# Performance work log

Measured on AMD Instinct MI355X. Metric: run time of the kernel, lower is better.

The kernel has to match this reference:

```python
import jax, jax.numpy as jnp
import numpy as np

B, S, W, V, E, H, T = 512, 512, 3, 100000, 128, 100, 64
PAD = 0


def setup_inputs() -> dict:
    key = jax.random.key(0)
    ks = jax.random.split(key, 10)
    inputs = jax.random.randint(ks[0], (B, S, W), 0, V)          # word feature ids
    tags = jax.random.randint(ks[1], (B, S), 0, T)
    emb_table = jax.random.normal(ks[2], (V, E), jnp.float32) * 0.1
    W1 = jax.random.normal(ks[3], (E, H), jnp.float32) * (1.0 / np.sqrt(E))
    b1 = jnp.zeros((H,), jnp.float32)
    W2 = jax.random.normal(ks[4], (H, T), jnp.float32) * (1.0 / np.sqrt(H))
    b2 = jnp.zeros((T,), jnp.float32)
    start_trans = jax.random.uniform(ks[5], (T,), jnp.float32, -0.1, 0.1)
    end_trans = jax.random.uniform(ks[6], (T,), jnp.float32, -0.1, 0.1)
    transitions = jax.random.uniform(ks[7], (T, T), jnp.float32, -0.1, 0.1)
    return {"inputs": inputs, "tags": tags, "emb_table": emb_table,
            "W1": W1, "b1": b1, "W2": W2, "b2": b2,
            "start_trans": start_trans, "end_trans": end_trans,
            "transitions": transitions}


def reference(inputs, tags, emb_table, W1, b1, W2, b2,
              start_trans, end_trans, transitions):
    # mask: token is real if any word feature != padding_idx. [S,B] (time-major)
    mask = (jnp.sum(inputs != PAD, axis=-1) != 0).T
    # Emission scorer (dropout disabled = eval/deterministic)
    emb = jnp.take(emb_table, inputs, axis=0).sum(axis=2)        # [B,S,E]
    h = jnp.tanh(emb @ W1 + b1)                                  # [B,S,H]
    em = (h @ W2 + b2).transpose(1, 0, 2)                        # [S,B,T]
    tags_t = tags.T                                              # [S,B]
    maskf = mask.astype(em.dtype)
    b_idx = jnp.arange(em.shape[1])

    # ---- numerator: score of the gold tag path ----
    score = start_trans[tags_t[0]] + em[0, b_idx, tags_t[0]]     # [B]
    trans_sc = transitions[tags_t[:-1], tags_t[1:]]              # [S-1,B]
    em_sc = jnp.take_along_axis(em[1:], tags_t[1:, :, None], axis=2)[..., 0]
    score = score + jnp.sum((trans_sc + em_sc) * maskf[1:], axis=0)
    seq_ends = jnp.sum(mask.astype(jnp.int32), axis=0) - 1       # [B]
    last_tags = tags_t[seq_ends, b_idx]
    numerator = score + end_trans[last_tags]

    # ---- denominator: log partition via forward algorithm (log-semiring scan) ----
    alpha0 = start_trans[None, :] + em[0]                        # [B,T]

    def step(alpha, x):
        em_t, m_t = x                                            # [B,T], [B]
        nxt = jax.nn.logsumexp(
            alpha[:, :, None] + transitions[None, :, :] + em_t[:, None, :],
            axis=1)                                              # [B,T]
        return jnp.where(m_t[:, None], nxt, alpha), None

    alpha, _ = jax.lax.scan(step, alpha0, (em[1:], mask[1:]))
    denominator = jax.nn.logsumexp(alpha + end_trans[None, :], axis=1)

    # loss = -log-likelihood, per batch element (reduce=False)
    return denominator - numerator
```

## Files before the change

kernel.cpp:

```cpp
#include <hip/hip_runtime.h>

#define B_ 512
#define S_ 512
#define E_ 128
#define H_ 100
#define T_ 64
#define V_ 100000
#define BS_ (B_*S_)

typedef __attribute__((ext_vector_type(8))) short bf16x8;
typedef __attribute__((ext_vector_type(4))) float f32x4;
typedef _Float16 h2 __attribute__((ext_vector_type(2)));
union U16x4 { uint4 u; bf16x8 s; };

__device__ __forceinline__ unsigned f2bf1(float x){
    unsigned u = __float_as_uint(x);
    return (u + 0x7FFFu + ((u>>16)&1u)) >> 16;
}
__device__ __forceinline__ float bf2f(unsigned short h){
    return __uint_as_float(((unsigned)h)<<16);
}
__device__ __forceinline__ float rfl_f(float x){
    return __uint_as_float(__builtin_amdgcn_readfirstlane(__float_as_uint(x)));
}
__device__ __forceinline__ unsigned addpack3(unsigned a, unsigned b, unsigned c){
    float lo = __uint_as_float(a<<16) + __uint_as_float(b<<16) + __uint_as_float(c<<16);
    float hi = __uint_as_float(a&0xFFFF0000u) + __uint_as_float(b&0xFFFF0000u)
             + __uint_as_float(c&0xFFFF0000u);
    return f2bf1(lo) | (f2bf1(hi)<<16);
}
__device__ __forceinline__ float fdot2h(unsigned u, h2 e, float c){
    h2 p; __builtin_memcpy(&p, &u, 4);
#if __has_builtin(__builtin_amdgcn_fdot2)
    return __builtin_amdgcn_fdot2(p, e, c, false);
#else
    return fmaf((float)p.x, (float)e.x, fmaf((float)p.y, (float)e.y, c));
#endif
}
__device__ __forceinline__ float dpp_xor1(float x){
    return __int_as_float(__builtin_amdgcn_mov_dpp(__float_as_int(x), 0xB1, 0xF, 0xF, true));
}
__device__ __forceinline__ float dpp_xor2(float x){
    return __int_as_float(__builtin_amdgcn_mov_dpp(__float_as_int(x), 0x4E, 0xF, 0xF, true));
}

__global__ __launch_bounds__(256) void prep_tbl(
    const float* __restrict__ tbl, uint2* __restrict__ tblh)
{
    int idx = blockIdx.x*256 + threadIdx.x;
    if (idx < (V_*E_)/4) {
        float4 v = ((const float4*)tbl)[idx];
        uint2 o;
        o.x = f2bf1(v.x) | (f2bf1(v.y)<<16);
        o.y = f2bf1(v.z) | (f2bf1(v.w)<<16);
        tblh[idx] = o;
    }
}

__global__ __launch_bounds__(64) void prep_w(
    const float* __restrict__ W1, const float* __restrict__ W2,
    uint4* __restrict__ W1f, uint4* __restrict__ W2f)
{
    const int idx = blockIdx.x*64 + threadIdx.x;
    if (idx < 7*4*64) {
        int lane = idx & 63, kt = (idx>>6)&3, nt = idx>>8;
        int n = nt*16 + (lane&15);
        int kb = kt*32 + (lane>>4)*8;
        unsigned wv[4];
        #pragma unroll
        for (int p = 0; p < 4; ++p) {
            float v0 = (n < H_) ? W1[(kb+2*p  )*H_ + n] : 0.f;
            float v1 = (n < H_) ? W1[(kb+2*p+1)*H_ + n] : 0.f;
            wv[p] = f2bf1(v0) | (f2bf1(v1) << 16);
        }
        W1f[idx] = make_uint4(wv[0],wv[1],wv[2],wv[3]);
    } else {
        int id2 = idx - 7*4*64;
        int lane = id2 & 63, kt = (id2>>6)&3, nt = id2>>8;
        int n = nt*16 + (lane&15);
        int kb = kt*32 + (lane>>4)*8;
        unsigned wv[4];
        #pragma unroll
        for (int p = 0; p < 4; ++p) {
            int k0 = kb+2*p, k1 = kb+2*p+1;
            float v0 = (k0 < H_) ? W2[k0*T_ + n] : 0.f;
            float v1 = (k1 < H_) ? W2[k1*T_ + n] : 0.f;
            wv[p] = f2bf1(v0) | (f2bf1(v1) << 16);
        }
        W2f[id2] = make_uint4(wv[0],wv[1],wv[2],wv[3]);
    }
}

__global__ __launch_bounds__(128)
__attribute__((amdgpu_waves_per_eu(1, 1)))
void fused_kernel(
    const int* __restrict__ inputs, const int* __restrict__ tags,
    const unsigned short* __restrict__ tblh,
    const float* __restrict__ b1, const float* __restrict__ b2,
    const uint4* __restrict__ W1f, const uint4* __restrict__ W2f,
    const float* __restrict__ start_trans, const float* __restrict__ end_trans,
    const float* __restrict__ trans, float* __restrict__ out)
{
    __shared__ uint4 sW1f[1792];
    __shared__ uint4 sW2f[1024];
    __shared__ __align__(16) unsigned short ring[2][4][512];
    __shared__ uint4 sA2[2][256];
    __shared__ __align__(16) _Float16 pbufH[2][T_];
    __shared__ float pubB[T_];
    __shared__ float fnum[2];
    __shared__ int   icnt[2];
    __shared__ float lsB_sh;

    const int b   = blockIdx.x;
    const int tid = threadIdx.x;
    const int w   = tid >> 6;
    const int j   = tid & 63;
    const int col = j & 15;
    const int hi  = j >> 4;
    const int rowin = hi * 4;
    const int qg  = j >> 2;
    const int qm  = j & 3;
    const bool qb0 = (j & 1) != 0;
    const bool qb1 = (j & 2) != 0;
    const int* tags_b = tags + b*S_;
    const int* in_b   = inputs + (size_t)b*S_*3;

    for (int i = tid; i < 1792; i += 128) sW1f[i] = W1f[i];
    for (int i = tid; i < 1024; i += 128) sW2f[i] = W2f[i];

    unsigned long long mball[4];
    #pragma unroll
    for (int g4 = 0; g4 < 4; ++g4) {
        int t = (w*4 + g4)*64 + j;
        int a0 = in_b[t*3+0], a1 = in_b[t*3+1], a2 = in_b[t*3+2];
        mball[g4] = __ballot((a0 | a1 | a2) != 0);
    }
    int cnt = 0;
    #pragma unroll
    for (int g4 = 0; g4 < 4; ++g4) cnt += __popcll(mball[g4]);
    if (j == 0) icnt[w] = cnt;
    if (w == 0) mball[0] &= ~1ull;

    __syncthreads();

    float bv1[7], bv2[4];
    #pragma unroll
    for (int nt = 0; nt < 7; ++nt) { int n = nt*16+col; bv1[nt] = (n < H_) ? b1[n] : 0.f; }
    #pragma unroll
    for (int nt2 = 0; nt2 < 4; ++nt2) bv2[nt2] = b2[nt2*16+col];

    h2 E2[32];
    #pragma unroll
    for (int o = 0; o < 4; ++o)
        #pragma unroll
        for (int i = 0; i < 8; ++i) {
            int r0, c0, r1, c1;
            if (w == 0) { r0 = 16*qm + 2*i; c0 = 4*qg + o; r1 = r0 + 1; c1 = c0; }
            else        { r0 = 4*qg + o; c0 = 16*qm + 2*i; r1 = r0; c1 = c0 + 1; }
            h2 e; e.x = (_Float16)__expf(trans[r0*T_ + c0]);
                  e.y = (_Float16)__expf(trans[r1*T_ + c1]);
            E2[o*8 + i] = e;
        }

    auto baseOf = [&](int p){ return w ? (480 - 16*p) : 16*p; };
    float np = 0.f;

    auto loadIdx = [&](int p, int& x, int& y, int& z){
        int t = baseOf(p) + col;
        x = in_b[t*3 + 0]; y = in_b[t*3 + 1]; z = in_b[t*3 + 2];
    };
    auto issueGathers = [&](int i0, int i1, int i2, uint4* g){
        const unsigned short* tr0 = tblh + (size_t)i0*E_;
        const unsigned short* tr1 = tblh + (size_t)i1*E_;
        const unsigned short* tr2 = tblh + (size_t)i2*E_;
        #pragma unroll
        for (int kt = 0; kt < 4; ++kt) {
            int off = kt*32 + hi*8;
            g[kt*3+0] = *(const uint4*)(tr0 + off);
            g[kt*3+1] = *(const uint4*)(tr1 + off);
            g[kt*3+2] = *(const uint4*)(tr2 + off);
        }
    };

    auto produce = [&](int p, const uint4* g){
        U16x4 a[4];
        #pragma unroll
        for (int kt = 0; kt < 4; ++kt)
            a[kt].u = make_uint4(
                addpack3(g[kt*3+0].x, g[kt*3+1].x, g[kt*3+2].x),
                addpack3(g[kt*3+0].y, g[kt*3+1].y, g[kt*3+2].y),
                addpack3(g[kt*3+0].z, g[kt*3+1].z, g[kt*3+2].z),
                addpack3(g[kt*3+0].w, g[kt*3+1].w, g[kt*3+2].w));

        f32x4 acc1[7];
        #pragma unroll
        for (int nt = 0; nt < 7; ++nt) {
            f32x4 c; c[0]=bv1[nt]; c[1]=bv1[nt]; c[2]=bv1[nt]; c[3]=bv1[nt];
            #pragma unroll
            for (int k = 0; k < 4; ++k) {
                U16x4 bfr; bfr.u = sW1f[(nt*4+k)*64 + j];
                c = __builtin_amdgcn_mfma_f32_16x16x32_bf16(a[k].s, bfr.s, c, 0,0,0);
            }
            acc1[nt] = c;
        }
        #pragma unroll
        for (int nt = 0; nt < 7; ++nt)
            #pragma unroll
            for (int rr = 0; rr < 4; ++rr) {
                float x = acc1[nt][rr];
                acc1[nt][rr] = 1.f - 2.f/(__expf(2.f*x)+1.f);
            }

        if (j >= 32) sA2[w][3*64 + j] = make_uint4(0,0,0,0);
        unsigned short* A2h = (unsigned short*)sA2[w];
        #pragma unroll
        for (int nt = 0; nt < 7; ++nt)
            #pragma unroll
            for (int rr = 0; rr < 4; ++rr) {
                int k2 = nt*16 + col;
                int kt2 = k2 >> 5, g2 = (k2>>3)&3, i2v = k2&7;
                int u4idx = kt2*64 + g2*16 + (rowin + rr);
                A2h[u4idx*8 + i2v] = (unsigned short)f2bf1(acc1[nt][rr]);
            }
        __builtin_amdgcn_wave_barrier();

        U16x4 a2[4];
        #pragma unroll
        for (int k = 0; k < 4; ++k) a2[k].u = sA2[w][k*64 + j];
        __builtin_amdgcn_wave_barrier();

        unsigned short* tbuf = (unsigned short*)sA2[w];
        #pragma unroll
        for (int nt2 = 0; nt2 < 4; ++nt2) {
            f32x4 c; c[0]=bv2[nt2]; c[1]=bv2[nt2]; c[2]=bv2[nt2]; c[3]=bv2[nt2];
            #pragma unroll
            for (int k = 0; k < 4; ++k) {
                U16x4 bfr; bfr.u = sW2f[(nt2*4+k)*64 + j];
                c = __builtin_amdgcn_mfma_f32_16x16x32_bf16(a2[k].s, bfr.s, c, 0,0,0);
            }
            #pragma unroll
            for (int rr = 0; rr < 4; ++rr)
                tbuf[(rowin+rr)*72 + nt2*16 + col] = (unsigned short)f2bf1(c[rr]);
        }
        __builtin_amdgcn_wave_barrier();

        {
            const int rl = j >> 2;
            const int ch = (j & 3) * 2;
            const uint4* t4 = (const uint4*)tbuf;
            uint4 u0 = t4[rl*9 + ch];
            uint4 u1 = t4[rl*9 + ch + 1];
            int row = baseOf(p) + rl;
            int grp = row >> 3;
            int kidx = w ? (63 - grp) : grp;
            uint4* dst = (uint4*)&ring[w][kidx & 3][(row & 7)*64];
            dst[ch]   = u0;
            dst[ch+1] = u1;
        }
        __builtin_amdgcn_wave_barrier();

        if (j < 16) {
            int t = baseOf(p) + j;
            if (t >= 1) {
                int word = (t >> 6) - w*4;
                if ((mball[word] >> (t & 63)) & 1ull) {
                    int tp = tags_b[t-1], tc = tags_b[t];
                    int grp = t >> 3;
                    int kidx = w ? (63 - grp) : grp;
                    np += trans[tp*T_ + tc] + bf2f(ring[w][kidx & 3][(t & 7)*64 + tc]);
                }
            }
        }
    };

    uint4 g[12];
    int i0, i1, i2, ni0, ni1, ni2;
    loadIdx(0, i0, i1, i2);
    issueGathers(i0, i1, i2, g);
    produce(0, g);
    float a, ls;
    if (w == 0) {
        if (j == 0) {
            int tag0 = tags_b[0];
            np += start_trans[tag0] + bf2f(ring[0][0][tag0]);
        }
        float x0v = start_trans[j] + bf2f(ring[0][0][j]);
        ls = rfl_f(x0v);
        a  = __expf(x0v - ls);
    } else {
        a  = __expf(end_trans[j]);
        ls = 0.f;
    }
    loadIdx(1, i0, i1, i2);
    issueGathers(i0, i1, i2, g);
    produce(1, g);
    loadIdx(2, i0, i1, i2);
    issueGathers(i0, i1, i2, g);
    loadIdx(3, ni0, ni1, ni2);

    float eg[8];
    #pragma unroll
    for (int s = 0; s < 8; ++s)
        eg[s] = __expf(bf2f(ring[w][0][(w ? (7-s) : s)*64 + j]));

    for (int p = 0; p < 16; ++p) {
        #pragma unroll
        for (int kk = 0; kk < 2; ++kk) {
            const int k = 2*p + kk;
            unsigned short raw16[8];
            if (k < 31) {
                const unsigned short* nxt = ring[w][(k+1) & 3];
                #pragma unroll
                for (int s = 0; s < 8; ++s)
                    raw16[s] = nxt[(w ? (7-s) : s)*64 + j];
            }
            const int ag = w ? (63 - k) : k;
            const unsigned mg = (unsigned)((mball[(ag>>3) - w*4] >> ((ag&7)*8)) & 0xFFull);

            #pragma unroll
            for (int s = 0; s < 8; ++s) {
                float wv = (w == 0) ? a : (eg[s] * a);
                pbufH[w][j] = (_Float16)(wv * 0.015625f);
                __builtin_amdgcn_wave_barrier();
                float sc   = rfl_f(a);
                float sinv = __builtin_amdgcn_rcpf(sc);
                float logs = __logf(sc);
                float keep = a * sinv;
                float dmul = ((w == 0) ? (eg[s] * sinv) : sinv) * 64.0f;

                const uint4* ph = (const uint4*)pbufH[w];
                uint4 U0 = ph[2*qm];
                uint4 U1 = ph[2*qm + 1];
                float p0, p1, p2, p3;
                p0 = fdot2h(U0.x, E2[ 0], 0.f);  p0 = fdot2h(U0.y, E2[ 1], p0);
                p0 = fdot2h(U0.z, E2[ 2], p0);   p0 = fdot2h(U0.w, E2[ 3], p0);
                p0 = fdot2h(U1.x, E2[ 4], p0);   p0 = fdot2h(U1.y, E2[ 5], p0);
                p0 = fdot2h(U1.z, E2[ 6], p0);   p0 = fdot2h(U1.w, E2[ 7], p0);
                p1 = fdot2h(U0.x, E2[ 8], 0.f);  p1 = fdot2h(U0.y, E2[ 9], p1);
                p1 = fdot2h(U0.z, E2[10], p1);   p1 = fdot2h(U0.w, E2[11], p1);
                p1 = fdot2h(U1.x, E2[12], p1);   p1 = fdot2h(U1.y, E2[13], p1);
                p1 = fdot2h(U1.z, E2[14], p1);   p1 = fdot2h(U1.w, E2[15], p1);
                p2 = fdot2h(U0.x, E2[16], 0.f);  p2 = fdot2h(U0.y, E2[17], p2);
                p2 = fdot2h(U0.z, E2[18], p2);   p2 = fdot2h(U0.w, E2[19], p2);
                p2 = fdot2h(U1.x, E2[20], p2);   p2 = fdot2h(U1.y, E2[21], p2);
                p2 = fdot2h(U1.z, E2[22], p2);   p2 = fdot2h(U1.w, E2[23], p2);
                p3 = fdot2h(U0.x, E2[24], 0.f);  p3 = fdot2h(U0.y, E2[25], p3);
                p3 = fdot2h(U0.z, E2[26], p3);   p3 = fdot2h(U0.w, E2[27], p3);
                p3 = fdot2h(U1.x, E2[28], p3);   p3 = fdot2h(U1.y, E2[29], p3);
                p3 = fdot2h(U1.z, E2[30], p3);   p3 = fdot2h(U1.w, E2[31], p3);

                float t0 = qb1 ? p2 : p0;
                float t1 = qb1 ? p3 : p1;
                float s0 = qb1 ? p0 : p2;
                float s1 = qb1 ? p1 : p3;
                t0 += dpp_xor2(s0);
                t1 += dpp_xor2(s1);
                float tt = qb0 ? t1 : t0;
                float ss = qb0 ? t0 : t1;
                float y  = tt + dpp_xor1(ss);

                float cand = y * dmul;
                const int bit = (w == 0) ? s : (7 - s);
                a = ((mg >> bit) & 1u) ? cand : keep;
                ls += logs;
                __builtin_amdgcn_wave_barrier();
            }
            if (k < 31) {
                #pragma unroll
                for (int s = 0; s < 8; ++s) eg[s] = __expf(bf2f(raw16[s]));
            }
        }
        if (p <= 13) produce(p + 2, g);
        if (p <= 12) {
            issueGathers(ni0, ni1, ni2, g);
            if (p <= 11) loadIdx(p + 4, ni0, ni1, ni2);
        }
    }

    #pragma unroll
    for (int off = 32; off >= 1; off >>= 1) np += __shfl_xor(np, off, 64);
    if (j == 0) fnum[w] = np;

    if (w == 1) {
        pubB[j] = a;
        if (j == 0) lsB_sh = ls;
    }
    __syncthreads();
    if (w == 0) {
        float x = a * pubB[j];
        #pragma unroll
        for (int off = 32; off >= 1; off >>= 1) x += __shfl_xor(x, off, 64);
        int mcount = icnt[0] + icnt[1];
        int se = mcount - 1; if (se < 0) se = 0;
        const int last_tag = tags_b[se];
        float numer = fnum[0] + fnum[1] + end_trans[last_tag];
        if (j == 0) out[b] = ls + lsB_sh + __logf(x) - numer;
    }
}

extern "C" void kernel_launch(void* const* d_in, const int* in_sizes, int n_in,
                              void* d_out, int out_size, void* d_ws, size_t ws_size,
                              hipStream_t stream) {
    const int*   inputs      = (const int*)  d_in[0];
    const int*   tags        = (const int*)  d_in[1];
    const float* emb_table   = (const float*)d_in[2];
    const float* W1          = (const float*)d_in[3];
    const float* b1          = (const float*)d_in[4];
    const float* W2          = (const float*)d_in[5];
    const float* b2          = (const float*)d_in[6];
    const float* start_trans = (const float*)d_in[7];
    const float* end_trans   = (const float*)d_in[8];
    const float* transitions = (const float*)d_in[9];
    float* out = (float*)d_out;

    unsigned short* tblh = (unsigned short*)d_ws;
    uint4* W1f = (uint4*)((char*)d_ws + (size_t)V_*E_*2);
    uint4* W2f = W1f + 7*4*64;

    prep_tbl<<<dim3((V_*E_/4 + 255)/256), dim3(256), 0, stream>>>(emb_table, (uint2*)tblh);
    prep_w<<<dim3((7*4*64 + 4*4*64)/64), dim3(64), 0, stream>>>(W1, W2, W1f, W2f);
    fused_kernel<<<dim3(B_), dim3(128), 0, stream>>>(
        inputs, tags, tblh, b1, b2, W1f, W2f,
        start_trans, end_trans, transitions, out);
}
```

Before: 222.7 us.

## Split fused CRF kernel into producer and consumer waves with LDS flag handshake

The block grows from two to four waves. Two producer waves compute emissions (gather plus both MLP layers) into a deeper 8-slot LDS ring, and two consumer waves run the forward and backward log-semiring scans. The waves synchronize through spin-waited shared-memory progress flags. Before, each wave interleaved its own emission production with its scan steps. The intent is to take emission latency off the serial scan critical path, at the cost of spin-wait overhead, extra LDS, and a register budget now capped by 256-thread launch bounds with two blocks per CU.

```diff
diff --git a/kernel.cpp b/kernel.cpp
--- a/kernel.cpp
+++ b/kernel.cpp
@@ -91,8 +91,7 @@
     }
 }
 
-__global__ __launch_bounds__(128)
-__attribute__((amdgpu_waves_per_eu(1, 1)))
+__global__ __launch_bounds__(256, 2)
 void fused_kernel(
     const int* __restrict__ inputs, const int* __restrict__ tags,
     const unsigned short* __restrict__ tblh,
@@ -103,232 +102,254 @@
 {
     __shared__ uint4 sW1f[1792];
     __shared__ uint4 sW2f[1024];
-    __shared__ __align__(16) unsigned short ring[2][4][512];
+    __shared__ __align__(16) unsigned short ring[2][8][512];
     __shared__ uint4 sA2[2][256];
     __shared__ __align__(16) _Float16 pbufH[2][T_];
     __shared__ float pubB[T_];
     __shared__ float fnum[2];
     __shared__ int   icnt[2];
     __shared__ float lsB_sh;
+    __shared__ int   prodF[2];
+    __shared__ int   consF[2];
 
     const int b   = blockIdx.x;
     const int tid = threadIdx.x;
-    const int w   = tid >> 6;
+    const int wid = tid >> 6;
     const int j   = tid & 63;
+    const int d   = wid & 1;
+    const bool isProd = wid >= 2;
     const int col = j & 15;
     const int hi  = j >> 4;
     const int rowin = hi * 4;
-    const int qg  = j >> 2;
-    const int qm  = j & 3;
-    const bool qb0 = (j & 1) != 0;
-    const bool qb1 = (j & 2) != 0;
     const int* tags_b = tags + b*S_;
     const int* in_b   = inputs + (size_t)b*S_*3;
 
-    for (int i = tid; i < 1792; i += 128) sW1f[i] = W1f[i];
-    for (int i = tid; i < 1024; i += 128) sW2f[i] = W2f[i];
+    for (int i = tid; i < 1792; i += 256) sW1f[i] = W1f[i];
+    for (int i = tid; i < 1024; i += 256) sW2f[i] = W2f[i];
+    if (tid == 0) { prodF[0] = prodF[1] = 0; consF[0] = consF[1] = 0; }
 
     unsigned long long mball[4];
     #pragma unroll
     for (int g4 = 0; g4 < 4; ++g4) {
-        int t = (w*4 + g4)*64 + j;
+        int t = (d*4 + g4)*64 + j;
         int a0 = in_b[t*3+0], a1 = in_b[t*3+1], a2 = in_b[t*3+2];
         mball[g4] = __ballot((a0 | a1 | a2) != 0);
     }
-    int cnt = 0;
-    #pragma unroll
-    for (int g4 = 0; g4 < 4; ++g4) cnt += __popcll(mball[g4]);
-    if (j == 0) icnt[w] = cnt;
-    if (w == 0) mball[0] &= ~1ull;
+    if (isProd) {
+        int cnt = 0;
+        #pragma unroll
+        for (int g4 = 0; g4 < 4; ++g4) cnt += __popcll(mball[g4]);
+        if (j == 0) icnt[d] = cnt;
+    }
 
     __syncthreads();
 
-    float bv1[7], bv2[4];
-    #pragma unroll
-    for (int nt = 0; nt < 7; ++nt) { int n = nt*16+col; bv1[nt] = (n < H_) ? b1[n] : 0.f; }
-    #pragma unroll
-    for (int nt2 = 0; nt2 < 4; ++nt2) bv2[nt2] = b2[nt2*16+col];
-
-    h2 E2[32];
-    #pragma unroll
-    for (int o = 0; o < 4; ++o)
-        #pragma unroll
-        for (int i = 0; i < 8; ++i) {
-            int r0, c0, r1, c1;
-            if (w == 0) { r0 = 16*qm + 2*i; c0 = 4*qg + o; r1 = r0 + 1; c1 = c0; }
-            else        { r0 = 4*qg + o; c0 = 16*qm + 2*i; r1 = r0; c1 = c0 + 1; }
-            h2 e; e.x = (_Float16)__expf(trans[r0*T_ + c0]);
-                  e.y = (_Float16)__expf(trans[r1*T_ + c1]);
-            E2[o*8 + i] = e;
-        }
-
-    auto baseOf = [&](int p){ return w ? (480 - 16*p) : 16*p; };
-    float np = 0.f;
-
-    auto loadIdx = [&](int p, int& x, int& y, int& z){
-        int t = baseOf(p) + col;
-        x = in_b[t*3 + 0]; y = in_b[t*3 + 1]; z = in_b[t*3 + 2];
-    };
-    auto issueGathers = [&](int i0, int i1, int i2, uint4* g){
-        const unsigned short* tr0 = tblh + (size_t)i0*E_;
-        const unsigned short* tr1 = tblh + (size_t)i1*E_;
-        const unsigned short* tr2 = tblh + (size_t)i2*E_;
-        #pragma unroll
-        for (int kt = 0; kt < 4; ++kt) {
-            int off = kt*32 + hi*8;
-            g[kt*3+0] = *(const uint4*)(tr0 + off);
-            g[kt*3+1] = *(const uint4*)(tr1 + off);
-            g[kt*3+2] = *(const uint4*)(tr2 + off);
-        }
-    };
-
-    auto produce = [&](int p, const uint4* g){
-        U16x4 a[4];
-        #pragma unroll
-        for (int kt = 0; kt < 4; ++kt)
-            a[kt].u = make_uint4(
-                addpack3(g[kt*3+0].x, g[kt*3+1].x, g[kt*3+2].x),
-                addpack3(g[kt*3+0].y, g[kt*3+1].y, g[kt*3+2].y),
-                addpack3(g[kt*3+0].z, g[kt*3+1].z, g[kt*3+2].z),
-                addpack3(g[kt*3+0].w, g[kt*3+1].w, g[kt*3+2].w));
-
-        f32x4 acc1[7];
-        #pragma unroll
-        for (int nt = 0; nt < 7; ++nt) {
-            f32x4 c; c[0]=bv1[nt]; c[1]=bv1[nt]; c[2]=bv1[nt]; c[3]=bv1[nt];
-            #pragma unroll
-            for (int k = 0; k < 4; ++k) {
-                U16x4 bfr; bfr.u = sW1f[(nt*4+k)*64 + j];
-                c = __builtin_amdgcn_mfma_f32_16x16x32_bf16(a[k].s, bfr.s, c, 0,0,0);
-            }
-            acc1[nt] = c;
-        }
-        #pragma unroll
-        for (int nt = 0; nt < 7; ++nt)
-            #pragma unroll
-            for (int rr = 0; rr < 4; ++rr) {
-                float x = acc1[nt][rr];
-                acc1[nt][rr] = 1.f - 2.f/(__expf(2.f*x)+1.f);
-            }
-
-        if (j >= 32) sA2[w][3*64 + j] = make_uint4(0,0,0,0);
-        unsigned short* A2h = (unsigned short*)sA2[w];
-        #pragma unroll
-        for (int nt = 0; nt < 7; ++nt)
-            #pragma unroll
-            for (int rr = 0; rr < 4; ++rr) {
-                int k2 = nt*16 + col;
-                int kt2 = k2 >> 5, g2 = (k2>>3)&3, i2v = k2&7;
-                int u4idx = kt2*64 + g2*16 + (rowin + rr);
-                A2h[u4idx*8 + i2v] = (unsigned short)f2bf1(acc1[nt][rr]);
-            }
-        __builtin_amdgcn_wave_barrier();
-
-        U16x4 a2[4];
-        #pragma unroll
-        for (int k = 0; k < 4; ++k) a2[k].u = sA2[w][k*64 + j];
-        __builtin_amdgcn_wave_barrier();
-
-        unsigned short* tbuf = (unsigned short*)sA2[w];
-        #pragma unroll
-        for (int nt2 = 0; nt2 < 4; ++nt2) {
-            f32x4 c; c[0]=bv2[nt2]; c[1]=bv2[nt2]; c[2]=bv2[nt2]; c[3]=bv2[nt2];
-            #pragma unroll
-            for (int k = 0; k < 4; ++k) {
-                U16x4 bfr; bfr.u = sW2f[(nt2*4+k)*64 + j];
-                c = __builtin_amdgcn_mfma_f32_16x16x32_bf16(a2[k].s, bfr.s, c, 0,0,0);
-            }
-            #pragma unroll
-            for (int rr = 0; rr < 4; ++rr)
-                tbuf[(rowin+rr)*72 + nt2*16 + col] = (unsigned short)f2bf1(c[rr]);
-        }
-        __builtin_amdgcn_wave_barrier();
-
-        {
-            const int rl = j >> 2;
-            const int ch = (j & 3) * 2;
-            const uint4* t4 = (const uint4*)tbuf;
-            uint4 u0 = t4[rl*9 + ch];
-            uint4 u1 = t4[rl*9 + ch + 1];
-            int row = baseOf(p) + rl;
-            int grp = row >> 3;
-            int kidx = w ? (63 - grp) : grp;
-            uint4* dst = (uint4*)&ring[w][kidx & 3][(row & 7)*64];
-            dst[ch]   = u0;
-            dst[ch+1] = u1;
-        }
-        __builtin_amdgcn_wave_barrier();
-
-        if (j < 16) {
-            int t = baseOf(p) + j;
-            if (t >= 1) {
-                int word = (t >> 6) - w*4;
-                if ((mball[word] >> (t & 63)) & 1ull) {
-                    int tp = tags_b[t-1], tc = tags_b[t];
-                    int grp = t >> 3;
-                    int kidx = w ? (63 - grp) : grp;
-                    np += trans[tp*T_ + tc] + bf2f(ring[w][kidx & 3][(t & 7)*64 + tc]);
+    auto baseOf = [&](int p){ return d ? (496 - 16*p) : 16*p; };
+
+    float aF = 0.f, lsF = 0.f;
+
+    if (isProd) {
+        float bv1[7], bv2[4];
+        #pragma unroll
+        for (int nt = 0; nt < 7; ++nt) { int n = nt*16+col; bv1[nt] = (n < H_) ? b1[n] : 0.f; }
+        #pragma unroll
+        for (int nt2 = 0; nt2 < 4; ++nt2) bv2[nt2] = b2[nt2*16+col];
+
+        auto loadIdx = [&](int p, int& x, int& y, int& z){
+            int t = baseOf(p) + col;
+            x = in_b[t*3 + 0]; y = in_b[t*3 + 1]; z = in_b[t*3 + 2];
+        };
+        auto issueGathers = [&](int i0, int i1, int i2, uint4* g){
+            const unsigned short* tr0 = tblh + (size_t)i0*E_;
+            const unsigned short* tr1 = tblh + (size_t)i1*E_;
+            const unsigned short* tr2 = tblh + (size_t)i2*E_;
+            #pragma unroll
+            for (int kt = 0; kt < 4; ++kt) {
+                int off = kt*32 + hi*8;
+                g[kt*3+0] = *(const uint4*)(tr0 + off);
+                g[kt*3+1] = *(const uint4*)(tr1 + off);
+                g[kt*3+2] = *(const uint4*)(tr2 + off);
+            }
+        };
+
+        uint4 g[12];
+        int i0, i1, i2;
+        float np = 0.f;
+        loadIdx(0, i0, i1, i2);
+        issueGathers(i0, i1, i2, g);
+
+        for (int p = 0; p < 16; ++p) {
+            U16x4 a4[4];
+            #pragma unroll
+            for (int kt = 0; kt < 4; ++kt)
+                a4[kt].u = make_uint4(
+                    addpack3(g[kt*3+0].x, g[kt*3+1].x, g[kt*3+2].x),
+                    addpack3(g[kt*3+0].y, g[kt*3+1].y, g[kt*3+2].y),
+                    addpack3(g[kt*3+0].z, g[kt*3+1].z, g[kt*3+2].z),
+                    addpack3(g[kt*3+0].w, g[kt*3+1].w, g[kt*3+2].w));
+            if (p < 15) { loadIdx(p+1, i0, i1, i2); issueGathers(i0, i1, i2, g); }
+
+            f32x4 acc1[7];
+            #pragma unroll
+            for (int nt = 0; nt < 7; ++nt) {
+                f32x4 c; c[0]=bv1[nt]; c[1]=bv1[nt]; c[2]=bv1[nt]; c[3]=bv1[nt];
+                #pragma unroll
+                for (int k = 0; k < 4; ++k) {
+                    U16x4 bfr; bfr.u = sW1f[(nt*4+k)*64 + j];
+                    c = __builtin_amdgcn_mfma_f32_16x16x32_bf16(a4[k].s, bfr.s, c, 0,0,0);
                 }
-            }
-        }
-    };
-
-    uint4 g[12];
-    int i0, i1, i2, ni0, ni1, ni2;
-    loadIdx(0, i0, i1, i2);
-    issueGathers(i0, i1, i2, g);
-    produce(0, g);
-    float a, ls;
-    if (w == 0) {
-        if (j == 0) {
-            int tag0 = tags_b[0];
-            np += start_trans[tag0] + bf2f(ring[0][0][tag0]);
-        }
-        float x0v = start_trans[j] + bf2f(ring[0][0][j]);
-        ls = rfl_f(x0v);
-        a  = __expf(x0v - ls);
+                acc1[nt] = c;
+            }
+            #pragma unroll
+            for (int nt = 0; nt < 7; ++nt)
+                #pragma unroll
+                for (int rr = 0; rr < 4; ++rr) {
+                    float x = acc1[nt][rr];
+                    acc1[nt][rr] = 1.f - 2.f/(__expf(2.f*x)+1.f);
+                }
+
+            if (j >= 32) sA2[d][3*64 + j] = make_uint4(0,0,0,0);
+            unsigned short* A2h = (unsigned short*)sA2[d];
+            #pragma unroll
+            for (int nt = 0; nt < 7; ++nt)
+                #pragma unroll
+                for (int rr = 0; rr < 4; ++rr) {
+                    int k2 = nt*16 + col;
+                    int kt2 = k2 >> 5, g2 = (k2>>3)&3, i2v = k2&7;
+                    int u4idx = kt2*64 + g2*16 + (rowin + rr);
+                    A2h[u4idx*8 + i2v] = (unsigned short)f2bf1(acc1[nt][rr]);
+                }
+            __builtin_amdgcn_wave_barrier();
+
+            U16x4 a2[4];
+            #pragma unroll
+            for (int k = 0; k < 4; ++k) a2[k].u = sA2[d][k*64 + j];
+            __builtin_amdgcn_wave_barrier();
+
+            unsigned short* tbuf = (unsigned short*)sA2[d];
+            #pragma unroll
+            for (int nt2 = 0; nt2 < 4; ++nt2) {
+                f32x4 c; c[0]=bv2[nt2]; c[1]=bv2[nt2]; c[2]=bv2[nt2]; c[3]=bv2[nt2];
+                #pragma unroll
+                for (int k = 0; k < 4; ++k) {
+                    U16x4 bfr; bfr.u = sW2f[(nt2*4+k)*64 + j];
+                    c = __builtin_amdgcn_mfma_f32_16x16x32_bf16(a2[k].s, bfr.s, c, 0,0,0);
+                }
+                #pragma unroll
+                for (int rr = 0; rr < 4; ++rr)
+                    tbuf[(rowin+rr)*72 + nt2*16 + col] = (unsigned short)f2bf1(c[rr]);
+            }
+            __builtin_amdgcn_wave_barrier();
+
+            if (p >= 4) {
+                volatile int* cf = &consF[d];
+                while (*cf < 2*p - 7) __builtin_amdgcn_s_sleep(1);
+                __asm__ volatile("" ::: "memory");
+            }
+            {
+                const int rl = j >> 2;
+                const int ch = (j & 3) * 2;
+                const uint4* t4 = (const uint4*)tbuf;
+                uint4 u0 = t4[rl*9 + ch];
+                uint4 u1 = t4[rl*9 + ch + 1];
+                int row = baseOf(p) + rl;
+                int grp = row >> 3;
+                int kidx = d ? (63 - grp) : grp;
+                uint4* dst = (uint4*)&ring[d][kidx & 7][(row & 7)*64];
+                dst[ch]   = u0;
+                dst[ch+1] = u1;
+            }
+            __asm__ volatile("s_waitcnt lgkmcnt(0)" ::: "memory");
+            if (j == 0) prodF[d] = 2*p + 2;
+            __builtin_amdgcn_wave_barrier();
+
+            if (j < 16) {
+                int t = baseOf(p) + j;
+                if (t >= 1) {
+                    int word = (t >> 6) - d*4;
+                    if ((mball[word] >> (t & 63)) & 1ull) {
+                        int tp = tags_b[t-1], tc = tags_b[t];
+                        int grp = t >> 3;
+                        int kidx = d ? (63 - grp) : grp;
+                        np += trans[tp*T_ + tc] + bf2f(ring[d][kidx & 7][(t & 7)*64 + tc]);
+                    }
+                }
+            }
+            if (d == 0 && p == 0 && j == 0) {
+                int tag0 = tags_b[0];
+                np += start_trans[tag0] + bf2f(ring[0][0][tag0]);
+            }
+        }
+
+        #pragma unroll
+        for (int off = 32; off >= 1; off >>= 1) np += __shfl_xor(np, off, 64);
+        if (j == 0) fnum[d] = np;
+
     } else {
-        a  = __expf(end_trans[j]);
-        ls = 0.f;
-    }
-    loadIdx(1, i0, i1, i2);
-    issueGathers(i0, i1, i2, g);
-    produce(1, g);
-    loadIdx(2, i0, i1, i2);
-    issueGathers(i0, i1, i2, g);
-    loadIdx(3, ni0, ni1, ni2);
-
-    float eg[8];
-    #pragma unroll
-    for (int s = 0; s < 8; ++s)
-        eg[s] = __expf(bf2f(ring[w][0][(w ? (7-s) : s)*64 + j]));
-
-    for (int p = 0; p < 16; ++p) {
-        #pragma unroll
-        for (int kk = 0; kk < 2; ++kk) {
-            const int k = 2*p + kk;
+        const int qg  = j >> 2;
+        const int qm  = j & 3;
+        const bool qb0 = (j & 1) != 0;
+        const bool qb1 = (j & 2) != 0;
+
+        h2 E2[32];
+        #pragma unroll
+        for (int o = 0; o < 4; ++o)
+            #pragma unroll
+            for (int i = 0; i < 8; ++i) {
+                int r0, c0, r1, c1;
+                if (d == 0) { r0 = 16*qm + 2*i; c0 = 4*qg + o; r1 = r0 + 1; c1 = c0; }
+                else        { r0 = 4*qg + o; c0 = 16*qm + 2*i; r1 = r0; c1 = c0 + 1; }
+                h2 e; e.x = (_Float16)__expf(trans[r0*T_ + c0]);
+                      e.y = (_Float16)__expf(trans[r1*T_ + c1]);
+                E2[o*8 + i] = e;
+            }
+        if (d == 0) mball[0] &= ~1ull;
+
+        volatile int* pf = &prodF[d];
+        while (*pf < 1) __builtin_amdgcn_s_sleep(1);
+        __asm__ volatile("" ::: "memory");
+
+        float a, ls;
+        if (d == 0) {
+            float x0v = start_trans[j] + bf2f(ring[0][0][j]);
+            ls = rfl_f(x0v);
+            a  = __expf(x0v - ls);
+        } else {
+            a  = __expf(end_trans[j]);
+            ls = 0.f;
+        }
+        float eg[8];
+        #pragma unroll
+        for (int s = 0; s < 8; ++s)
+            eg[s] = __expf(bf2f(ring[d][0][(d ? (7-s) : s)*64 + j]));
+
+        for (int k = 0; k < 32; ++k) {
             unsigned short raw16[8];
             if (k < 31) {
-                const unsigned short* nxt = ring[w][(k+1) & 3];
+                while (*pf < k + 2) __builtin_amdgcn_s_sleep(1);
+                __asm__ volatile("" ::: "memory");
+                const unsigned short* nxt = ring[d][(k+1) & 7];
                 #pragma unroll
                 for (int s = 0; s < 8; ++s)
-                    raw16[s] = nxt[(w ? (7-s) : s)*64 + j];
-            }
-            const int ag = w ? (63 - k) : k;
-            const unsigned mg = (unsigned)((mball[(ag>>3) - w*4] >> ((ag&7)*8)) & 0xFFull);
+                    raw16[s] = nxt[(d ? (7-s) : s)*64 + j];
+                __asm__ volatile("s_waitcnt lgkmcnt(0)" ::: "memory");
+                if (j == 0) consF[d] = k + 1;
+            }
+            const int ag = d ? (63 - k) : k;
+            const unsigned mg = (unsigned)((mball[(ag>>3) - d*4] >> ((ag&7)*8)) & 0xFFull);
 
             #pragma unroll
             for (int s = 0; s < 8; ++s) {
-                float wv = (w == 0) ? a : (eg[s] * a);
-                pbufH[w][j] = (_Float16)(wv * 0.015625f);
+                float wv = (d == 0) ? a : (eg[s] * a);
+                pbufH[d][j] = (_Float16)(wv * 0.015625f);
                 __builtin_amdgcn_wave_barrier();
                 float sc   = rfl_f(a);
                 float sinv = __builtin_amdgcn_rcpf(sc);
                 float logs = __logf(sc);
                 float keep = a * sinv;
-                float dmul = ((w == 0) ? (eg[s] * sinv) : sinv) * 64.0f;
-
-                const uint4* ph = (const uint4*)pbufH[w];
+                float dmul = ((d == 0) ? (eg[s] * sinv) : sinv) * 64.0f;
+
+                const uint4* ph = (const uint4*)pbufH[d];
                 uint4 U0 = ph[2*qm];
                 uint4 U1 = ph[2*qm + 1];
                 float p0, p1, p2, p3;
@@ -360,7 +381,7 @@
                 float y  = tt + dpp_xor1(ss);
 
                 float cand = y * dmul;
-                const int bit = (w == 0) ? s : (7 - s);
+                const int bit = (d == 0) ? s : (7 - s);
                 a = ((mg >> bit) & 1u) ? cand : keep;
                 ls += logs;
                 __builtin_amdgcn_wave_barrier();
@@ -370,31 +391,26 @@
                 for (int s = 0; s < 8; ++s) eg[s] = __expf(bf2f(raw16[s]));
             }
         }
-        if (p <= 13) produce(p + 2, g);
-        if (p <= 12) {
-            issueGathers(ni0, ni1, ni2, g);
-            if (p <= 11) loadIdx(p + 4, ni0, ni1, ni2);
-        }
-    }
-
-    #pragma unroll
-    for (int off = 32; off >= 1; off >>= 1) np += __shfl_xor(np, off, 64);
-    if (j == 0) fnum[w] = np;
-
-    if (w == 1) {
-        pubB[j] = a;
-        if (j == 0) lsB_sh = ls;
-    }
+
+        if (d == 1) {
+            pubB[j] = a;
+            if (j == 0) lsB_sh = ls;
+        } else {
+            aF = a; lsF = ls;
+        }
+    }
+
     __syncthreads();
-    if (w == 0) {
-        float x = a * pubB[j];
+
+    if (wid == 0) {
+        float x = aF * pubB[j];
         #pragma unroll
         for (int off = 32; off >= 1; off >>= 1) x += __shfl_xor(x, off, 64);
         int mcount = icnt[0] + icnt[1];
         int se = mcount - 1; if (se < 0) se = 0;
         const int last_tag = tags_b[se];
         float numer = fnum[0] + fnum[1] + end_trans[last_tag];
-        if (j == 0) out[b] = ls + lsB_sh + __logf(x) - numer;
+        if (j == 0) out[b] = lsF + lsB_sh + __logf(x) - numer;
     }
 }
 
@@ -419,7 +435,7 @@
 
     prep_tbl<<<dim3((V_*E_/4 + 255)/256), dim3(256), 0, stream>>>(emb_table, (uint2*)tblh);
     prep_w<<<dim3((7*4*64 + 4*4*64)/64), dim3(64), 0, stream>>>(W1, W2, W1f, W2f);
-    fused_kernel<<<dim3(B_), dim3(128), 0, stream>>>(
+    fused_kernel<<<dim3(B_), dim3(256), 0, stream>>>(
         inputs, tags, tblh, b1, b2, W1f, W2f,
         start_trans, end_trans, transitions, out);
 }
```

Result: faster. 204.0 us (-8.4%).
